# Kernel tuning notes

Measured on AMD Instinct MI355X. Metric: run time of the kernel, lower is better.

Reference implementation:

```python
import jax, jax.numpy as jnp
import numpy as np

EPS = 1e-5
SLOPE = 0.2


def _bn(x, g, b, m, v):
    # eval-mode BatchNorm1d over channel dim (last axis here)
    return (x - m) * (g * jax.lax.rsqrt(v + EPS)) + b


def _lrelu(x):
    return jnp.where(x >= 0, x, SLOPE * x)


def setup_inputs() -> dict:
    key = jax.random.key(0)
    ks = jax.random.split(key, 24)
    B, N = 16, 2048
    d = {
        "x_query": jax.random.normal(ks[0], (B, 2048), jnp.float32),
        "x_key": jax.random.normal(ks[1], (B, N, 512), jnp.float32),
        "W1": jax.random.normal(ks[2], (2048, 512), jnp.float32) * 0.02,
        "W2": jax.random.normal(ks[3], (512, 2048), jnp.float32) * 0.02,
        "W3": jax.random.normal(ks[4], (64, 512), jnp.float32) * 0.02,
        "W4": jax.random.normal(ks[5], (1, 64), jnp.float32) * 0.02,
    }
    for i, c in zip(range(4), (2048, 512, 64, 1)):
        d[f"g{i+1}"] = jax.random.uniform(ks[6 + 4 * i], (c,), jnp.float32, 0.5, 1.5)
        d[f"b{i+1}"] = jax.random.normal(ks[7 + 4 * i], (c,), jnp.float32) * 0.1
        d[f"m{i+1}"] = jax.random.normal(ks[8 + 4 * i], (c,), jnp.float32) * 0.1
        d[f"v{i+1}"] = jax.random.uniform(ks[9 + 4 * i], (c,), jnp.float32, 0.5, 1.5)
    return d


def reference(x_query, x_key, W1, W2, W3, W4,
              g1, b1, m1, v1, g2, b2, m2, v2,
              g3, b3, m3, v3, g4, b4, m4, v4):
    # values: [B, N, 2048]
    values = _lrelu(_bn(jnp.einsum('bnd,ed->bne', x_key, W1), g1, b1, m1, v1))
    features = values + x_query[:, None, :]
    s = _lrelu(_bn(jnp.einsum('bne,de->bnd', features, W2), g2, b2, m2, v2))
    s = _lrelu(_bn(jnp.einsum('bnd,kd->bnk', s, W3), g3, b3, m3, v3))
    s = _lrelu(_bn(jnp.einsum('bnk,ok->bno', s, W4), g4, b4, m4, v4))  # [B,N,1]
    scores = jax.nn.softmax(s[..., 0], axis=1)  # [B,N]
    feature = jnp.einsum('bne,bn->be', values, scores)  # softmax-weighted sum pool
    return feature
```

## Files before the change

### kernel.cpp

```cpp
#include <hip/hip_runtime.h>
#include <hip/hip_bf16.h>

typedef __bf16 bf16x8 __attribute__((ext_vector_type(8)));
typedef float f32x4 __attribute__((ext_vector_type(4)));
typedef __attribute__((address_space(3))) void lds_void_t;
typedef __attribute__((address_space(1))) void gbl_void_t;

#define LRELU(x) ((x) >= 0.f ? (x) : 0.2f * (x))

__device__ __forceinline__ void gload16(void* lds_uniform, const void* gsrc) {
    __builtin_amdgcn_global_load_lds((const gbl_void_t*)gsrc, (lds_void_t*)lds_uniform,
                                     16, 0, 0);
}

__device__ __forceinline__ unsigned short f2u(float f) {
    __hip_bfloat16 h = __float2bfloat16(f);
    return reinterpret_cast<unsigned short&>(h);
}

__global__ void cvt_f32_bf16(const float* __restrict__ in,
                             __hip_bfloat16* __restrict__ out, int n4) {
    int stride = gridDim.x * blockDim.x;
    for (int i = blockIdx.x * blockDim.x + threadIdx.x; i < n4; i += stride) {
        float4 v = reinterpret_cast<const float4*>(in)[i];
        ushort4 o;
        o.x = f2u(v.x); o.y = f2u(v.y); o.z = f2u(v.z); o.w = f2u(v.w);
        reinterpret_cast<ushort4*>(out)[i] = o;
    }
}

template <int N, int K, int MODE>
__global__ __launch_bounds__(512, 2)
void gemm256(const __hip_bfloat16* __restrict__ A,
             const __hip_bfloat16* __restrict__ Bw,
             const float* __restrict__ xq,
             __hip_bfloat16* __restrict__ out,
             const float* __restrict__ Gg, const float* __restrict__ Gb,
             const float* __restrict__ Gm, const float* __restrict__ Gv) {
    __shared__ __hip_bfloat16 sm[3 * 16384];

    const int nwg = gridDim.x;
    const int cpx = nwg >> 3;
    const int bid = blockIdx.x;
    const int orig = (bid & 7) * cpx + (bid >> 3);
    constexpr int NCB = N / 256;
    const int rowblk = orig / NCB;
    const int colblk = orig % NCB;
    const int row0 = rowblk * 256, col0 = colblk * 256;

    const int tid = threadIdx.x;
    const int lane = tid & 63;
    const int wv = tid >> 6;
    const int wm = wv >> 2, wn = wv & 3;
    const int lr = lane & 15, kg = lane >> 4;

    const int srow = tid >> 2;
    const int sc = tid & 3;
    const int kch = ((sc ^ ((srow >> 1) & 3)) << 3);
    const __hip_bfloat16* As0 = A + (size_t)(row0 + srow) * K + kch;
    const __hip_bfloat16* As1 = A + (size_t)(row0 + 128 + srow) * K + kch;
    const __hip_bfloat16* Bs0 = Bw + (size_t)(col0 + srow) * K + kch;
    const __hip_bfloat16* Bs1 = Bw + (size_t)(col0 + 128 + srow) * K + kch;

    auto STAGE = [&](int b, int k0) {
        __hip_bfloat16* la = sm + b * 16384 + wv * 512;
        __hip_bfloat16* lb = la + 8192;
        gload16(la,        As0 + k0);
        gload16(la + 4096, As1 + k0);
        gload16(lb,        Bs0 + k0);
        gload16(lb + 4096, Bs1 + k0);
    };

    const int f = (lr >> 1) & 3;
    const int koff = ((kg ^ f) << 3);
    const int aoff = (wm * 128 + lr) * 32 + koff;
    const int boff = 8192 + (wn * 64 + lr) * 32 + koff;

    f32x4 acc[8][4];
#pragma unroll
    for (int i = 0; i < 8; ++i)
#pragma unroll
        for (int j = 0; j < 4; ++j) acc[i][j] = (f32x4){0.f, 0.f, 0.f, 0.f};

    constexpr int nt = K / 32;
    STAGE(0, 0);
    STAGE(1, 32);

    for (int t = 0; t < nt; ++t) {
        if (t + 2 < nt) {
            STAGE((t + 2) % 3, (t + 2) * 32);
            asm volatile("s_waitcnt vmcnt(8)" ::: "memory");
        } else if (t + 1 < nt) {
            asm volatile("s_waitcnt vmcnt(4)" ::: "memory");
        } else {
            asm volatile("s_waitcnt vmcnt(0)" ::: "memory");
        }
        __builtin_amdgcn_s_barrier();
        __builtin_amdgcn_sched_barrier(0);

        const __hip_bfloat16* base = sm + (t % 3) * 16384;
        bf16x8 af[8], bfr[4];
#pragma unroll
        for (int i = 0; i < 8; ++i)
            af[i] = *reinterpret_cast<const bf16x8*>(base + aoff + i * 512);
#pragma unroll
        for (int j = 0; j < 4; ++j)
            bfr[j] = *reinterpret_cast<const bf16x8*>(base + boff + j * 512);

        __builtin_amdgcn_s_setprio(1);
#pragma unroll
        for (int i = 0; i < 8; ++i)
#pragma unroll
            for (int j = 0; j < 4; ++j)
                acc[i][j] = __builtin_amdgcn_mfma_f32_16x16x32_bf16(af[i], bfr[j], acc[i][j], 0, 0, 0);
        __builtin_amdgcn_s_setprio(0);
        __builtin_amdgcn_sched_barrier(0);
        __builtin_amdgcn_s_barrier();
    }

    const int bq = row0 >> 11;
#pragma unroll
    for (int j = 0; j < 4; ++j) {
        const int c = col0 + wn * 64 + j * 16 + lr;
        const float scl = Gg[c] * rsqrtf(Gv[c] + 1e-5f);
        const float tcn = Gb[c] - Gm[c] * scl;
        float xqv = 0.f;
        if constexpr (MODE == 1) xqv = xq[bq * 2048 + c];
#pragma unroll
        for (int i = 0; i < 8; ++i) {
            const int r = row0 + wm * 128 + i * 16 + kg * 4;
#pragma unroll
            for (int rI = 0; rI < 4; ++rI) {
                float val = acc[i][j][rI] * scl + tcn;
                val = LRELU(val) + xqv;
                out[(size_t)(r + rI) * N + c] = __float2bfloat16(val);
            }
        }
    }
}

__global__ __launch_bounds__(256)
void gemm3_l4(const __hip_bfloat16* __restrict__ A,
              const __hip_bfloat16* __restrict__ W3b,
              const float* __restrict__ W4,
              const float* __restrict__ g3, const float* __restrict__ b3,
              const float* __restrict__ m3, const float* __restrict__ v3,
              const float* __restrict__ g4, const float* __restrict__ b4,
              const float* __restrict__ m4, const float* __restrict__ v4,
              float* __restrict__ logits) {
    const int lane = threadIdx.x & 63;
    const int wv = threadIdx.x >> 6;
    const int row0 = blockIdx.x * 128 + wv * 32;
    const int lr = lane & 15, kg = lane >> 4;

    f32x4 acc[2][4];
#pragma unroll
    for (int i = 0; i < 2; ++i)
#pragma unroll
        for (int j = 0; j < 4; ++j) acc[i][j] = (f32x4){0.f, 0.f, 0.f, 0.f};

    for (int k = 0; k < 512; k += 32) {
        const int kk = k + kg * 8;
        bf16x8 a[2], b[4];
#pragma unroll
        for (int i = 0; i < 2; ++i)
            a[i] = *reinterpret_cast<const bf16x8*>(A + (size_t)(row0 + i * 16 + lr) * 512 + kk);
#pragma unroll
        for (int j = 0; j < 4; ++j)
            b[j] = *reinterpret_cast<const bf16x8*>(W3b + (size_t)(j * 16 + lr) * 512 + kk);
#pragma unroll
        for (int i = 0; i < 2; ++i)
#pragma unroll
            for (int j = 0; j < 4; ++j)
                acc[i][j] = __builtin_amdgcn_mfma_f32_16x16x32_bf16(a[i], b[j], acc[i][j], 0, 0, 0);
    }

    const float sc4 = g4[0] * rsqrtf(v4[0] + 1e-5f);
    const float tc4 = b4[0] - m4[0] * sc4;
#pragma unroll
    for (int i = 0; i < 2; ++i) {
        float t[4] = {0.f, 0.f, 0.f, 0.f};
#pragma unroll
        for (int j = 0; j < 4; ++j) {
            const int c = j * 16 + lr;
            const float sc = g3[c] * rsqrtf(v3[c] + 1e-5f);
            const float tc = b3[c] - m3[c] * sc;
            const float w4c = W4[c];
#pragma unroll
            for (int rI = 0; rI < 4; ++rI) {
                float v = acc[i][j][rI] * sc + tc;
                t[rI] += LRELU(v) * w4c;
            }
        }
#pragma unroll
        for (int m = 1; m < 16; m <<= 1)
#pragma unroll
            for (int rI = 0; rI < 4; ++rI) t[rI] += __shfl_xor(t[rI], m, 64);
        if (lr == 0) {
#pragma unroll
            for (int rI = 0; rI < 4; ++rI) {
                float lg = t[rI] * sc4 + tc4;
                logits[row0 + i * 16 + kg * 4 + rI] = LRELU(lg);
            }
        }
    }
}

__global__ void softmax2048(const float* __restrict__ logits, float* __restrict__ scores) {
    __shared__ float sh[2048];
    __shared__ float red[256];
    const int b = blockIdx.x, tid = threadIdx.x;
    float lmax = -1e30f;
#pragma unroll
    for (int it = 0; it < 8; ++it) {
        const int n = tid + it * 256;
        float v = logits[b * 2048 + n];
        sh[n] = v;
        lmax = fmaxf(lmax, v);
    }
    red[tid] = lmax;
    __syncthreads();
    for (int s = 128; s > 0; s >>= 1) {
        if (tid < s) red[tid] = fmaxf(red[tid], red[tid + s]);
        __syncthreads();
    }
    const float gmax = red[0];
    __syncthreads();
    float lsum = 0.f;
#pragma unroll
    for (int it = 0; it < 8; ++it) {
        const int n = tid + it * 256;
        float e = expf(sh[n] - gmax);
        sh[n] = e;
        lsum += e;
    }
    red[tid] = lsum;
    __syncthreads();
    for (int s = 128; s > 0; s >>= 1) {
        if (tid < s) red[tid] += red[tid + s];
        __syncthreads();
    }
    const float inv = 1.f / red[0];
#pragma unroll
    for (int it = 0; it < 8; ++it) {
        const int n = tid + it * 256;
        scores[b * 2048 + n] = sh[n] * inv;
    }
}

__global__ void pool_partial(const __hip_bfloat16* __restrict__ feats,
                             const float* __restrict__ scores,
                             float* __restrict__ partial) {
    const int b = blockIdx.y, nc = blockIdx.x;
    const int e0 = threadIdx.x * 8;
    float acc[8] = {0, 0, 0, 0, 0, 0, 0, 0};
    const size_t base = ((size_t)b * 2048 + nc * 64) * 2048;
    for (int i = 0; i < 64; ++i) {
        const float sc = scores[b * 2048 + nc * 64 + i];
        bf16x8 v = *reinterpret_cast<const bf16x8*>(feats + base + (size_t)i * 2048 + e0);
#pragma unroll
        for (int j = 0; j < 8; ++j) acc[j] += sc * (float)v[j];
    }
    float* p = partial + ((size_t)(b * 32 + nc)) * 2048 + e0;
#pragma unroll
    for (int j = 0; j < 8; ++j) p[j] = acc[j];
}

__global__ void pool_reduce(const float* __restrict__ partial,
                            const float* __restrict__ xq,
                            float* __restrict__ out) {
    const int i = blockIdx.x * blockDim.x + threadIdx.x;
    const int b = i >> 11, e = i & 2047;
    float s = 0.f;
#pragma unroll
    for (int nc = 0; nc < 32; ++nc) s += partial[((size_t)(b * 32 + nc)) * 2048 + e];
    out[i] = s - xq[i];
}

extern "C" void kernel_launch(void* const* d_in, const int* in_sizes, int n_in,
                              void* d_out, int out_size, void* d_ws, size_t ws_size,
                              hipStream_t stream) {
    const float* xq = (const float*)d_in[0];
    const float* xk = (const float*)d_in[1];
    const float* W1 = (const float*)d_in[2];
    const float* W2 = (const float*)d_in[3];
    const float* W3 = (const float*)d_in[4];
    const float* W4 = (const float*)d_in[5];
    const float* g1 = (const float*)d_in[6], *b1 = (const float*)d_in[7];
    const float* m1 = (const float*)d_in[8], *v1 = (const float*)d_in[9];
    const float* g2 = (const float*)d_in[10], *b2 = (const float*)d_in[11];
    const float* m2 = (const float*)d_in[12], *v2 = (const float*)d_in[13];
    const float* g3 = (const float*)d_in[14], *b3 = (const float*)d_in[15];
    const float* m3 = (const float*)d_in[16], *v3 = (const float*)d_in[17];
    const float* g4 = (const float*)d_in[18], *b4 = (const float*)d_in[19];
    const float* m4 = (const float*)d_in[20], *v4 = (const float*)d_in[21];

    const int M = 32768;

    char* ws = (char*)d_ws;
    size_t off = 0;
    auto alloc = [&](size_t bytes) {
        void* p = ws + off;
        off += (bytes + 255) & ~(size_t)255;
        return p;
    };
    __hip_bfloat16* xkb   = (__hip_bfloat16*)alloc((size_t)M * 512 * 2);
    __hip_bfloat16* w1b   = (__hip_bfloat16*)alloc((size_t)2048 * 512 * 2);
    __hip_bfloat16* w2b   = (__hip_bfloat16*)alloc((size_t)512 * 2048 * 2);
    __hip_bfloat16* w3b   = (__hip_bfloat16*)alloc((size_t)64 * 512 * 2);
    __hip_bfloat16* featb = (__hip_bfloat16*)alloc((size_t)M * 2048 * 2);
    __hip_bfloat16* s2b   = (__hip_bfloat16*)alloc((size_t)M * 512 * 2);
    float* logits         = (float*)alloc((size_t)M * 4);
    float* scores         = (float*)alloc((size_t)16 * 2048 * 4);
    float* partial        = (float*)alloc((size_t)16 * 32 * 2048 * 4);

    cvt_f32_bf16<<<4096, 256, 0, stream>>>(xk, xkb, M * 512 / 4);
    cvt_f32_bf16<<<1024, 256, 0, stream>>>(W1, w1b, 2048 * 512 / 4);
    cvt_f32_bf16<<<1024, 256, 0, stream>>>(W2, w2b, 512 * 2048 / 4);
    cvt_f32_bf16<<<32, 256, 0, stream>>>(W3, w3b, 64 * 512 / 4);

    gemm256<2048, 512, 1><<<1024, 512, 0, stream>>>(
        xkb, w1b, xq, featb, g1, b1, m1, v1);

    gemm256<512, 2048, 2><<<256, 512, 0, stream>>>(
        featb, w2b, nullptr, s2b, g2, b2, m2, v2);

    gemm3_l4<<<256, 256, 0, stream>>>(s2b, w3b, W4,
                                      g3, b3, m3, v3, g4, b4, m4, v4, logits);

    softmax2048<<<16, 256, 0, stream>>>(logits, scores);

    pool_partial<<<dim3(32, 16), 256, 0, stream>>>(featb, scores, partial);
    pool_reduce<<<128, 256, 0, stream>>>(partial, xq, (float*)d_out);
}
```

Baseline: 245.0 us.

## Issue prefetch after the barrier to drop the second per-iteration barrier in GEMM

The triple-buffered GEMM main loop now waits for stage t, passes a single barrier, and only then issues global-to-LDS loads for stage t+2 into the buffer read in iteration t-1. This removes the trailing barrier and sched_barrier from each iteration. It also drops the s_setprio hints around the MFMA block. Separately, the epilogue precomputes the BN scale, shift and query offsets per column and then loops rows outermost, so stores to each row are grouped together. The gain comes from less synchronization per k-step, at the cost of relying on the single barrier to protect buffer reuse and losing the priority boost.

```diff
diff --git a/kernel.cpp b/kernel.cpp
--- a/kernel.cpp
+++ b/kernel.cpp
@@ -62,11 +62,13 @@
     const __hip_bfloat16* Bs0 = Bw + (size_t)(col0 + srow) * K + kch;
     const __hip_bfloat16* Bs1 = Bw + (size_t)(col0 + 128 + srow) * K + kch;
 
-    auto STAGE = [&](int b, int k0) {
+    auto STAGE_A = [&](int b, int k0) {
         __hip_bfloat16* la = sm + b * 16384 + wv * 512;
-        __hip_bfloat16* lb = la + 8192;
         gload16(la,        As0 + k0);
         gload16(la + 4096, As1 + k0);
+    };
+    auto STAGE_B = [&](int b, int k0) {
+        __hip_bfloat16* lb = sm + b * 16384 + 8192 + wv * 512;
         gload16(lb,        Bs0 + k0);
         gload16(lb + 4096, Bs1 + k0);
     };
@@ -83,14 +85,11 @@
         for (int j = 0; j < 4; ++j) acc[i][j] = (f32x4){0.f, 0.f, 0.f, 0.f};
 
     constexpr int nt = K / 32;
-    STAGE(0, 0);
-    STAGE(1, 32);
+    STAGE_A(0, 0);  STAGE_B(0, 0);
+    STAGE_A(1, 32); STAGE_B(1, 32);
 
     for (int t = 0; t < nt; ++t) {
-        if (t + 2 < nt) {
-            STAGE((t + 2) % 3, (t + 2) * 32);
-            asm volatile("s_waitcnt vmcnt(8)" ::: "memory");
-        } else if (t + 1 < nt) {
+        if (t + 1 < nt) {
             asm volatile("s_waitcnt vmcnt(4)" ::: "memory");
         } else {
             asm volatile("s_waitcnt vmcnt(0)" ::: "memory");
@@ -100,6 +99,11 @@
 
         const __hip_bfloat16* base = sm + (t % 3) * 16384;
         bf16x8 af[8], bfr[4];
+
+        if (t + 2 < nt) {
+            STAGE_A((t + 2) % 3, (t + 2) * 32);
+            STAGE_B((t + 2) % 3, (t + 2) * 32);
+        }
 #pragma unroll
         for (int i = 0; i < 8; ++i)
             af[i] = *reinterpret_cast<const bf16x8*>(base + aoff + i * 512);
@@ -107,33 +111,33 @@
         for (int j = 0; j < 4; ++j)
             bfr[j] = *reinterpret_cast<const bf16x8*>(base + boff + j * 512);
 
-        __builtin_amdgcn_s_setprio(1);
 #pragma unroll
         for (int i = 0; i < 8; ++i)
 #pragma unroll
             for (int j = 0; j < 4; ++j)
                 acc[i][j] = __builtin_amdgcn_mfma_f32_16x16x32_bf16(af[i], bfr[j], acc[i][j], 0, 0, 0);
-        __builtin_amdgcn_s_setprio(0);
-        __builtin_amdgcn_sched_barrier(0);
-        __builtin_amdgcn_s_barrier();
     }
 
     const int bq = row0 >> 11;
+    float scl[4], tcn[4], xqv[4];
 #pragma unroll
     for (int j = 0; j < 4; ++j) {
         const int c = col0 + wn * 64 + j * 16 + lr;
-        const float scl = Gg[c] * rsqrtf(Gv[c] + 1e-5f);
-        const float tcn = Gb[c] - Gm[c] * scl;
-        float xqv = 0.f;
-        if constexpr (MODE == 1) xqv = xq[bq * 2048 + c];
-#pragma unroll
-        for (int i = 0; i < 8; ++i) {
-            const int r = row0 + wm * 128 + i * 16 + kg * 4;
-#pragma unroll
-            for (int rI = 0; rI < 4; ++rI) {
-                float val = acc[i][j][rI] * scl + tcn;
-                val = LRELU(val) + xqv;
-                out[(size_t)(r + rI) * N + c] = __float2bfloat16(val);
+        scl[j] = Gg[c] * rsqrtf(Gv[c] + 1e-5f);
+        tcn[j] = Gb[c] - Gm[c] * scl[j];
+        xqv[j] = (MODE == 1) ? xq[bq * 2048 + c] : 0.f;
+    }
+#pragma unroll
+    for (int i = 0; i < 8; ++i) {
+#pragma unroll
+        for (int rI = 0; rI < 4; ++rI) {
+            const int r = row0 + wm * 128 + i * 16 + kg * 4 + rI;
+            const size_t rowoff = (size_t)r * N + col0 + wn * 64 + lr;
+#pragma unroll
+            for (int j = 0; j < 4; ++j) {
+                float val = acc[i][j][rI] * scl[j] + tcn[j];
+                val = LRELU(val) + xqv[j];
+                out[rowoff + j * 16] = __float2bfloat16(val);
             }
         }
     }
```

Measured after the change: 221.5 us. 1.11x faster.
